# Performance work log

Measured on AMD Instinct MI355X. Metric: run time of the kernel, lower is better.

Reference implementation:

```python
import jax, jax.numpy as jnp
import numpy as np

# Dimensions (see shape_source)
B, D, Q, M = 2, 1024, 1024, 1024
K = Q + M                      # klen = mlen + qlen
N_HEAD, D_HEAD = 16, 64        # n_head * d_head == d_model
D_INNER = 4096
LOCAL_SIZE = 1000              # Attention: self.local_size or 1000
EPS = 1e-5                     # F.layer_norm default eps


def setup_inputs() -> dict:
    key = jax.random.key(0)
    ks = jax.random.split(key, 12)
    z = jax.random.normal(ks[0], (B, D, Q), jnp.float32)
    z_hist = jax.random.normal(ks[1], (B, D, M), jnp.float32)
    u = jax.random.normal(ks[2], (B, 3 * N_HEAD * D_HEAD, K), jnp.float32) * 0.1
    # sinusoidal relative position embedding (PositionalEmbedding), positions K-1..0
    inv_freq = 1.0 / (10000.0 ** (jnp.arange(0, D, 2, dtype=jnp.float32) / D))
    pos_seq = jnp.arange(K - 1, -1, -1, dtype=jnp.float32)
    sinusoid = inv_freq[:, None] * pos_seq[None, :]  # (D/2, K)
    pos_emb = jnp.concatenate([jnp.sin(sinusoid), jnp.cos(sinusoid)], axis=0)[None]  # (1, D, K)
    s = 0.02
    W_qkv = jax.random.normal(ks[3], (3 * N_HEAD * D_HEAD, D), jnp.float32) * s
    W_r = jax.random.normal(ks[4], (N_HEAD * D_HEAD, D), jnp.float32) * s
    r_w_bias = jax.random.uniform(ks[5], (N_HEAD, D_HEAD), jnp.float32, -0.05, 0.05)
    r_r_bias = jax.random.uniform(ks[6], (N_HEAD, D_HEAD), jnp.float32, -0.05, 0.05)
    W_o = jax.random.normal(ks[7], (D, N_HEAD * D_HEAD), jnp.float32) * s
    b_o = jnp.zeros((D,), jnp.float32)
    W_ff1 = jax.random.normal(ks[8], (D_INNER, D), jnp.float32) * s
    b_ff1 = jnp.zeros((D_INNER,), jnp.float32)
    W_ff2 = jax.random.normal(ks[9], (D, D_INNER), jnp.float32) * s
    b_ff2 = jnp.zeros((D,), jnp.float32)
    return dict(z=z, z_hist=z_hist, u=u, pos_emb=pos_emb, W_qkv=W_qkv, W_r=W_r,
                r_w_bias=r_w_bias, r_r_bias=r_r_bias, W_o=W_o, b_o=b_o,
                W_ff1=W_ff1, b_ff1=b_ff1, W_ff2=W_ff2, b_ff2=b_ff2)


def _ln(x, axis):
    # F.layer_norm without affine params
    mu = jnp.mean(x, axis=axis, keepdims=True)
    var = jnp.var(x, axis=axis, keepdims=True)
    return (x - mu) / jnp.sqrt(var + EPS)


def _rel_shift(x):
    # Transformer-XL relative shift: pad left on key dim, reinterpret, drop row.
    b, n, q, k = x.shape
    x = jnp.pad(x, ((0, 0), (0, 0), (0, 0), (1, 0)))
    x = x.reshape(b, n, k + 1, q)
    return x[:, :, 1:, :].reshape(b, n, q, k)


def reference(z, z_hist, u, pos_emb, W_qkv, W_r, r_w_bias, r_r_bias, W_o, b_o,
              W_ff1, b_ff1, W_ff2, b_ff2):
    scale = 1.0 / (D_HEAD ** 0.5)
    # ---- Attention (post-LN, Conv1d kernel=1 == pointwise matmul) ----
    cat = jnp.concatenate([z_hist, z], axis=2)                 # (B, D, K)
    w_heads = jnp.einsum('od,bdk->bok', W_qkv, cat) + u        # (B, 3*n*dh, K)
    q_h, k_h, v_h = jnp.split(w_heads, 3, axis=1)
    q_h = q_h[:, :, -Q:].reshape(B, N_HEAD, D_HEAD, Q)
    k_h = k_h.reshape(B, N_HEAD, D_HEAD, K)
    v_h = v_h.reshape(B, N_HEAD, D_HEAD, K)
    r_k = jnp.einsum('od,dk->ok', W_r, pos_emb[0]).reshape(N_HEAD, D_HEAD, K)
    AC = jnp.einsum('bndi,bndj->bnij', q_h + r_w_bias[:, :, None], k_h)
    BD = _rel_shift(jnp.einsum('bndi,ndj->bnij', q_h + r_r_bias[:, :, None], r_k))
    score = (AC + BD) * scale                                  # (B, n, Q, K)
    causal = jnp.triu(jnp.ones((Q, K), bool), k=1 + M)         # future tokens
    local = jnp.tril(jnp.ones((Q, K), bool), k=M - LOCAL_SIZE)  # beyond local window
    mask = causal | local
    score = jnp.where(mask[None, None], -jnp.inf, score)
    prob = jax.nn.softmax(score, axis=-1)
    attn_vec = jnp.einsum('bnij,bndj->bndi', prob, v_h).reshape(B, N_HEAD * D_HEAD, Q)
    attn_out = jnp.einsum('od,bdq->boq', W_o, attn_vec) + b_o[None, :, None]
    out = _ln(attn_out + z, axis=1)                            # LN over d_model (dim=1)
    # ---- FFN (operates token-major) ----
    h = out.transpose(0, 2, 1)                                 # (B, Q, D)
    ff = jnp.maximum(h @ W_ff1.T + b_ff1, 0.0) @ W_ff2.T + b_ff2
    y = _ln(ff + h, axis=-1)
    return y.transpose(0, 2, 1)                                # (B, D, Q)
```

## Files before the change

### kernel.cpp

```cpp
#include <hip/hip_runtime.h>

#define D_MODEL 1024
#define QLEN 1024

typedef __bf16 bf16x8 __attribute__((ext_vector_type(8)));
typedef __bf16 bf16x4 __attribute__((ext_vector_type(4)));
typedef float f32x4 __attribute__((ext_vector_type(4)));

__device__ __forceinline__ void gload16(const void* g, void* l) {
    __builtin_amdgcn_global_load_lds(
        (const __attribute__((address_space(1))) void*)g,
        (__attribute__((address_space(3))) void*)l, 16, 0, 0);
}

__device__ __forceinline__ void gemm_core8(
    __bf16* __restrict__ smA, __bf16* __restrict__ smB,
    const __bf16* __restrict__ A, const __bf16* __restrict__ Bt,
    float* __restrict__ C, __bf16* __restrict__ Cb,
    const float* __restrict__ U, const __bf16* __restrict__ Ub,
    const float* __restrict__ bias,
    int K, int lda, int ldb, int ldC, int ldU, int relu, int m0, int n0)
{
    const int t = threadIdx.x;
    const int lane = t & 63, w = t >> 6;
    const int l15 = lane & 15, lg = lane >> 4;
    const int wm = w >> 2, wn = w & 3;
    const int srow = lane >> 3, cpr = lane & 7;
    const int NK = K >> 6;
    const int SZ = 128 * 64;

    #define STAGE(buf, kt)                                                                   \
    {                                                                                        \
        int k0s = (kt) * 64;                                                                 \
        _Pragma("unroll")                                                                    \
        for (int i = 0; i < 2; ++i) {                                                        \
            int r = w * 16 + i * 8 + srow;                                                   \
            int c = cpr ^ (r & 7);                                                           \
            gload16(&A[(long long)(m0 + r) * lda + k0s + c * 8],                             \
                    &smA[(buf) * SZ + (w * 16 + i * 8) * 64]);                               \
            gload16(&Bt[(long long)(n0 + r) * ldb + k0s + c * 8],                            \
                    &smB[(buf) * SZ + (w * 16 + i * 8) * 64]);                               \
        }                                                                                    \
    }

    f32x4 acc[4][2] = {};
    STAGE(0, 0);

    for (int kt = 0; kt < NK; ++kt) {
        const int cb = kt & 1;
        if (kt + 1 < NK) {
            STAGE(cb ^ 1, kt + 1);
            asm volatile("s_waitcnt vmcnt(4)" ::: "memory");
        } else {
            asm volatile("s_waitcnt vmcnt(0)" ::: "memory");
        }
        __builtin_amdgcn_sched_barrier(0);
        __builtin_amdgcn_s_barrier();

        #pragma unroll
        for (int kk = 0; kk < 2; ++kk) {
            bf16x8 bfr[2];
            #pragma unroll
            for (int nt = 0; nt < 2; ++nt) {
                int nr = wn * 32 + nt * 16 + l15;
                bfr[nt] = *(const bf16x8*)&smB[cb * SZ + nr * 64 + (((kk * 4 + lg) ^ (nr & 7)) * 8)];
            }
            #pragma unroll
            for (int mt = 0; mt < 4; ++mt) {
                int mr = wm * 64 + mt * 16 + l15;
                bf16x8 afr = *(const bf16x8*)&smA[cb * SZ + mr * 64 + (((kk * 4 + lg) ^ (mr & 7)) * 8)];
                #pragma unroll
                for (int nt = 0; nt < 2; ++nt)
                    acc[mt][nt] = __builtin_amdgcn_mfma_f32_16x16x32_bf16(afr, bfr[nt], acc[mt][nt], 0, 0, 0);
            }
        }
        asm volatile("s_waitcnt lgkmcnt(0)" ::: "memory");
        __builtin_amdgcn_sched_barrier(0);
        __builtin_amdgcn_s_barrier();
    }
    #undef STAGE

    #pragma unroll
    for (int mt = 0; mt < 4; ++mt) {
        #pragma unroll
        for (int nt = 0; nt < 2; ++nt) {
            #pragma unroll
            for (int rg = 0; rg < 4; ++rg) {
                int m = m0 + wm * 64 + mt * 16 + lg * 4 + rg;
                int n = n0 + wn * 32 + nt * 16 + l15;
                float v = acc[mt][nt][rg];
                if (U)    v += U[(long long)m * ldU + n];
                if (Ub)   v += (float)Ub[(long long)m * ldU + n];
                if (bias) v += bias[n];
                if (relu) v = fmaxf(v, 0.0f);
                if (Cb) Cb[(long long)m * ldC + n] = (__bf16)v;
                else    C [(long long)m * ldC + n] = v;
            }
        }
    }
}

template<int KSPLIT>
__global__ __launch_bounds__(512) void gemm_bf16_k(
    const __bf16* __restrict__ A, const __bf16* __restrict__ Bt,
    float* __restrict__ C0, float* __restrict__ C1,
    float* __restrict__ C2, float* __restrict__ C3,
    __bf16* __restrict__ Cb,
    const float* __restrict__ U, const __bf16* __restrict__ Ub,
    const float* __restrict__ bias,
    int K, int lda, int ldb, int ldC, int ldU, int relu)
{
    __shared__ __bf16 SM[32768];
    int yb = blockIdx.y;
    int half = 0;
    if (KSPLIT > 1) { half = yb & (KSPLIT - 1); yb /= KSPLIT; }
    const int Keff = K / KSPLIT;
    A  += (long long)half * Keff;
    Bt += (long long)half * Keff;
    float* C = (half == 0) ? C0 : (half == 1) ? C1 : (half == 2) ? C2 : C3;
    if (half) { bias = nullptr; U = nullptr; Ub = nullptr; }
    gemm_core8(SM, SM + 16384, A, Bt, C, Cb, U, Ub, bias,
               Keff, lda, ldb, ldC, ldU, relu, yb * 128, blockIdx.x * 128);
}

__global__ __launch_bounds__(512) void gemm_fused3(
    const __bf16* __restrict__ cat_t, const __bf16* __restrict__ Wqkvb,
    __bf16* __restrict__ qkT, const __bf16* __restrict__ uqkT,
    __bf16* __restrict__ wh_v, const float* __restrict__ uv,
    const __bf16* __restrict__ pos_t, const __bf16* __restrict__ Wrb,
    __bf16* __restrict__ rkT)
{
    __shared__ __bf16 SM[32768];
    int bid = blockIdx.x;
    if (bid < 512) {
        int zz = bid >> 8, rem = bid & 255, y = rem >> 4, x = rem & 15;
        gemm_core8(SM, SM + 16384,
                   cat_t + (long long)zz * 2097152, Wqkvb,
                   nullptr, qkT + (long long)zz * 4194304,
                   nullptr, uqkT + (long long)zz * 4194304, nullptr,
                   1024, 1024, 1024, 2048, 2048, 0, y * 128, x * 128);
    } else if (bid < 768) {
        int l = bid - 512, zz = l >> 7, rem = l & 127, y = rem >> 4, x = rem & 15;
        gemm_core8(SM, SM + 16384,
                   Wqkvb + 2048 * 1024, cat_t + (long long)zz * 2097152,
                   nullptr, wh_v + (long long)zz * 2097152,
                   uv + (long long)zz * 6291456, nullptr, nullptr,
                   1024, 1024, 1024, 2048, 2048, 0, y * 128, x * 128);
    } else {
        int l = bid - 768, y = l >> 3, x = l & 7;
        gemm_core8(SM, SM + 16384,
                   pos_t + 960 * 1024, Wrb,
                   nullptr, rkT, nullptr, nullptr, nullptr,
                   1024, 1024, 1024, 1024, 0, 0, y * 128, x * 128);
    }
}

__global__ __launch_bounds__(256) void prep_all(
    const float* __restrict__ Wqkv, __bf16* __restrict__ Wqkvb,
    const float* __restrict__ Wr,   __bf16* __restrict__ Wrb,
    const float* __restrict__ Wo,   __bf16* __restrict__ Wob,
    const float* __restrict__ Wff1, __bf16* __restrict__ Wff1b,
    const float* __restrict__ Wff2, __bf16* __restrict__ Wff2b,
    const float* __restrict__ zh, const float* __restrict__ z, __bf16* __restrict__ cat_t,
    const float* __restrict__ pos, __bf16* __restrict__ pos_t,
    const float* __restrict__ u, __bf16* __restrict__ uqkT)
{
    __shared__ float ts[32][33];
    int bid = blockIdx.x;
    const int t = threadIdx.x;
    if (bid < 13312) {
        long long i = ((long long)bid * 256 + t) * 4;
        const float* s; __bf16* dd;
        if (i < 3145728)                    { s = Wqkv + i; dd = Wqkvb + i; }
        else if ((i -= 3145728) < 1048576)  { s = Wr + i;   dd = Wrb + i; }
        else if ((i -= 1048576) < 1048576)  { s = Wo + i;   dd = Wob + i; }
        else if ((i -= 1048576) < 4194304)  { s = Wff1 + i; dd = Wff1b + i; }
        else { i -= 4194304;                  s = Wff2 + i; dd = Wff2b + i; }
        float4 v = *(const float4*)s;
        bf16x4 o = { (__bf16)v.x, (__bf16)v.y, (__bf16)v.z, (__bf16)v.w };
        *(bf16x4*)dd = o;
        return;
    }
    bid -= 13312;
    const float* S; __bf16* D; int R, Cc, bx, by;
    if (bid < 2048) {
        int zz = bid >> 10, r2 = bid & 1023;
        S = zh + (long long)zz * 1048576; D = cat_t + (long long)zz * 2097152;
        R = 1024; Cc = 1024; bx = r2 & 31; by = r2 >> 5;
    } else if (bid < 4096) {
        int l = bid - 2048; int zz = l >> 10, r2 = l & 1023;
        S = z + (long long)zz * 1048576; D = cat_t + 1048576 + (long long)zz * 2097152;
        R = 1024; Cc = 1024; bx = r2 & 31; by = r2 >> 5;
    } else if (bid < 6144) {
        int l = bid - 4096;
        S = pos; D = pos_t; R = 1024; Cc = 2048; bx = l & 63; by = l >> 6;
    } else if (bid < 14336) {
        int l = bid - 6144; int zz = l >> 12, r2 = l & 4095;
        S = u + (long long)zz * 6291456; D = uqkT + (long long)zz * 4194304;
        R = 2048; Cc = 2048; bx = r2 & 63; by = r2 >> 6;
    } else {
        int l = bid - 14336;
        int i = (l * 256 + t) * 4;
        bf16x4 zv = { (__bf16)0.f, (__bf16)0.f, (__bf16)0.f, (__bf16)0.f };
        *(bf16x4*)&pos_t[2048 * 1024 + i] = zv;
        return;
    }
    int r0 = by * 32, c0 = bx * 32;
    int tr = t >> 5, tc = t & 31;
    #pragma unroll
    for (int p = 0; p < 4; ++p)
        ts[tr + p * 8][tc] = S[(long long)(r0 + tr + p * 8) * Cc + c0 + tc];
    __syncthreads();
    #pragma unroll
    for (int p = 0; p < 4; ++p)
        D[(long long)(c0 + tr + p * 8) * R + r0 + tc] = (__bf16)ts[tc][tr + p * 8];
}

__global__ __launch_bounds__(256) void attn_mfma(
    const __bf16* __restrict__ QKT, const __bf16* __restrict__ WHV,
    const __bf16* __restrict__ RKT,
    const float* __restrict__ rwb, const float* __restrict__ rrb,
    __bf16* __restrict__ AVt)
{
    __shared__ __bf16 SM[38144];
    __bf16* KT0 = SM;
    __bf16* KT1 = SM + 4096;
    __bf16* VS0 = SM + 8192;
    __bf16* VS1 = SM + 12288;
    __bf16* RT  = SM + 16384;
    __bf16* PS  = SM + 28672;
    __bf16* BT  = SM + 32768;

    const int d = blockIdx.x;
    const int xcd = d & 7, idx = d >> 3;
    const int qt = idx & 15;
    const int gq = xcd + 8 * (idx >> 4);
    const int b = gq >> 4, n = gq & 15;
    const int i0 = qt * 64;

    const int t = threadIdx.x;
    const int lane = t & 63, w = t >> 6;
    const int l15 = lane & 15, lg = lane >> 4;
    const int fco = n * 64;

    const __bf16* qkb = QKT + (long long)b * (2048 * 2048);
    const __bf16* vb  = WHV + (long long)b * (1024 * 2048) + (long long)fco * 2048;
    __bf16* BTw = BT + w * 1344;

    #pragma unroll
    for (int pp = 0; pp < 2; ++pp) {
        int cid = pp * 256 + t;
        int q = cid >> 3, s = cid & 7, c = s ^ (q & 7);
        bf16x8 qv = *(const bf16x8*)&qkb[(long long)(1024 + i0 + q) * 2048 + fco + c * 8];
        bf16x8 ow, orr;
        #pragma unroll
        for (int e = 0; e < 8; ++e) {
            float qf = (float)qv[e];
            ow[e]  = (__bf16)(qf + rwb[fco + c * 8 + e]);
            orr[e] = (__bf16)(qf + rrb[fco + c * 8 + e]);
        }
        *(bf16x8*)&PS[q * 64 + s * 8] = ow;
        *(bf16x8*)&VS0[q * 64 + s * 8] = orr;
    }
    __syncthreads();

    #define LDF(buf, row, ch) (*(const bf16x8*)&(buf)[(row) * 64 + ((((ch) ^ ((row) & 7))) * 8)])

    const int mrow = w * 16 + l15;
    bf16x8 qw0 = LDF(PS, mrow, lg), qw1 = LDF(PS, mrow, lg + 4);
    bf16x8 qr0 = LDF(VS0, mrow, lg), qr1 = LDF(VS0, mrow, lg + 4);
    asm volatile("s_waitcnt lgkmcnt(0)" ::: "memory");
    __builtin_amdgcn_sched_barrier(0);
    __builtin_amdgcn_s_barrier();

    #pragma unroll
    for (int pp = 0; pp < 2; ++pp) {
        int cid = pp * 256 + t;
        int r = cid >> 3, s = cid & 7, c = s ^ (r & 7);
        gload16(&qkb[(long long)(i0 + r) * 2048 + 1024 + fco + c * 8], &KT0[(pp * 32 + w * 8) * 64]);
        gload16(&vb[(long long)r * 2048 + i0 + c * 8], &VS0[(pp * 32 + w * 8) * 64]);
    }
    #pragma unroll
    for (int pp = 0; pp < 6; ++pp) {
        int cid = pp * 256 + t;
        int r = cid >> 3, s = cid & 7, c = s ^ (r & 7);
        gload16(&RKT[(long long)r * 1024 + fco + c * 8], &RT[(pp * 32 + w * 8) * 64]);
    }
    asm volatile("s_waitcnt vmcnt(0)" ::: "memory");
    __builtin_amdgcn_sched_barrier(0);
    __builtin_amdgcn_s_barrier();

    const bf16x8 ones = { (__bf16)1.f, (__bf16)1.f, (__bf16)1.f, (__bf16)1.f,
                          (__bf16)1.f, (__bf16)1.f, (__bf16)1.f, (__bf16)1.f };

    f32x4 O0 = {}, O1 = {}, O2 = {}, O3 = {};
    float rm[4] = {-1e30f, -1e30f, -1e30f, -1e30f};
    float rl[4] = {0.f, 0.f, 0.f, 0.f};
    int cur = 0;

    for (int kt = 0; kt <= 16; ++kt) {
        __bf16* KTc = cur ? KT1 : KT0;
        __bf16* VSc = cur ? VS1 : VS0;
        __bf16* KTn = cur ? KT0 : KT1;
        __bf16* VSn = cur ? VS0 : VS1;
        const int rbase = (kt % 3) * 64;

        if (kt < 16) {
            int j0n = i0 + (kt + 1) * 64;
            #pragma unroll
            for (int pp = 0; pp < 2; ++pp) {
                int cid = pp * 256 + t;
                int r = cid >> 3, s = cid & 7, c = s ^ (r & 7);
                gload16(&qkb[(long long)(j0n + r) * 2048 + 1024 + fco + c * 8], &KTn[(pp * 32 + w * 8) * 64]);
                gload16(&vb[(long long)r * 2048 + j0n + c * 8], &VSn[(pp * 32 + w * 8) * 64]);
            }
            int rb = kt * 64 + 128;
            int lb = ((kt + 2) % 3) * 64;
            #pragma unroll
            for (int pp = 0; pp < 2; ++pp) {
                int cid = pp * 256 + t;
                int r = cid >> 3, s = cid & 7, c = s ^ (r & 7);
                gload16(&RKT[(long long)(rb + r) * 1024 + fco + c * 8], &RT[(lb + pp * 32 + w * 8) * 64]);
            }
        }
        __builtin_amdgcn_sched_barrier(0);

        __builtin_amdgcn_s_setprio(1);
        #pragma unroll
        for (int k5 = 0; k5 < 5; ++k5) {
            int pr = (3 - w + k5) * 16 + l15;
            int lr = rbase + pr; if (lr >= 192) lr -= 192;
            const __bf16* rrow = &RT[lr * 64];
            f32x4 cc = {};
            cc = __builtin_amdgcn_mfma_f32_16x16x32_bf16(qr0, *(const bf16x8*)&rrow[((lg ^ (pr & 7)) * 8)], cc, 0, 0, 0);
            cc = __builtin_amdgcn_mfma_f32_16x16x32_bf16(qr1, *(const bf16x8*)&rrow[(((lg + 4) ^ (pr & 7)) * 8)], cc, 0, 0, 0);
            #pragma unroll
            for (int rg = 0; rg < 4; ++rg)
                BTw[(lg * 4 + rg) * 84 + k5 * 16 + l15] = (__bf16)cc[rg];
        }
        __builtin_amdgcn_s_setprio(0);

        f32x4 cc4[4];
        __builtin_amdgcn_s_setprio(1);
        #pragma unroll
        for (int nt = 0; nt < 4; ++nt) {
            int jr = nt * 16 + l15;
            f32x4 cc = {};
            cc = __builtin_amdgcn_mfma_f32_16x16x32_bf16(qw0, LDF(KTc, jr, lg), cc, 0, 0, 0);
            cc = __builtin_amdgcn_mfma_f32_16x16x32_bf16(qw1, LDF(KTc, jr, lg + 4), cc, 0, 0, 0);
            cc4[nt] = cc;
        }
        __builtin_amdgcn_s_setprio(0);

        const bool bnd = (kt < 2) | (kt == 16);
        float sv[4][4];
        if (!bnd) {
            #pragma unroll
            for (int nt = 0; nt < 4; ++nt) {
                int jr = nt * 16 + l15;
                #pragma unroll
                for (int rg = 0; rg < 4; ++rg) {
                    int r4 = lg * 4 + rg;
                    sv[nt][rg] = (cc4[nt][rg] + (float)BTw[r4 * 84 + jr - r4 + 15]) * 0.125f;
                }
            }
        } else {
            #pragma unroll
            for (int nt = 0; nt < 4; ++nt) {
                int jr = nt * 16 + l15;
                #pragma unroll
                for (int rg = 0; rg < 4; ++rg) {
                    int r4 = lg * 4 + rg;
                    int dji = jr - (w * 16 + r4);
                    float s = (cc4[nt][rg] + (float)BTw[r4 * 84 + jr - r4 + 15]) * 0.125f;
                    bool valid = (kt == 0) ? (dji >= 25)
                               : (kt == 1) ? (dji >= -39)
                               : (dji <= 0);
                    sv[nt][rg] = valid ? s : -1e30f;
                }
            }
        }

        float lmax[4];
        bool need = false;
        #pragma unroll
        for (int rg = 0; rg < 4; ++rg) {
            lmax[rg] = fmaxf(fmaxf(sv[0][rg], sv[1][rg]), fmaxf(sv[2][rg], sv[3][rg]));
            need = need || (lmax[rg] > rm[rg] + 8.0f);
        }
        if (__any(need)) {
            #pragma unroll
            for (int rg = 0; rg < 4; ++rg) {
                float m = lmax[rg];
                m = fmaxf(m, __shfl_xor(m, 1, 16));
                m = fmaxf(m, __shfl_xor(m, 2, 16));
                m = fmaxf(m, __shfl_xor(m, 4, 16));
                m = fmaxf(m, __shfl_xor(m, 8, 16));
                float nm = fmaxf(rm[rg], m);
                float fac = __expf(rm[rg] - nm);
                rm[rg] = nm;
                rl[rg] *= fac;
                O0[rg] *= fac; O1[rg] *= fac; O2[rg] *= fac; O3[rg] *= fac;
            }
        }

        if (!bnd) {
            #pragma unroll
            for (int nt = 0; nt < 4; ++nt) {
                int jc = nt * 16 + l15;
                #pragma unroll
                for (int rg = 0; rg < 4; ++rg) {
                    float p = __expf(sv[nt][rg] - rm[rg]);
                    int row = w * 16 + lg * 4 + rg;
                    PS[row * 64 + (((jc >> 3) ^ (row & 7)) * 8) + (jc & 7)] = (__bf16)p;
                }
            }
        } else {
            #pragma unroll
            for (int nt = 0; nt < 4; ++nt) {
                int jc = nt * 16 + l15;
                #pragma unroll
                for (int rg = 0; rg < 4; ++rg) {
                    float p = (sv[nt][rg] > -1e29f) ? __expf(sv[nt][rg] - rm[rg]) : 0.0f;
                    int row = w * 16 + lg * 4 + rg;
                    PS[row * 64 + (((jc >> 3) ^ (row & 7)) * 8) + (jc & 7)] = (__bf16)p;
                }
            }
        }

        bf16x8 pa0 = LDF(PS, mrow, lg), pa1 = LDF(PS, mrow, lg + 4);
        f32x4 Os = {};
        __builtin_amdgcn_s_setprio(1);
        Os = __builtin_amdgcn_mfma_f32_16x16x32_bf16(pa0, ones, Os, 0, 0, 0);
        Os = __builtin_amdgcn_mfma_f32_16x16x32_bf16(pa1, ones, Os, 0, 0, 0);
        O0 = __builtin_amdgcn_mfma_f32_16x16x32_bf16(pa0, LDF(VSc,  0 + l15, lg),     O0, 0, 0, 0);
        O0 = __builtin_amdgcn_mfma_f32_16x16x32_bf16(pa1, LDF(VSc,  0 + l15, lg + 4), O0, 0, 0, 0);
        O1 = __builtin_amdgcn_mfma_f32_16x16x32_bf16(pa0, LDF(VSc, 16 + l15, lg),     O1, 0, 0, 0);
        O1 = __builtin_amdgcn_mfma_f32_16x16x32_bf16(pa1, LDF(VSc, 16 + l15, lg + 4), O1, 0, 0, 0);
        O2 = __builtin_amdgcn_mfma_f32_16x16x32_bf16(pa0, LDF(VSc, 32 + l15, lg),     O2, 0, 0, 0);
        O2 = __builtin_amdgcn_mfma_f32_16x16x32_bf16(pa1, LDF(VSc, 32 + l15, lg + 4), O2, 0, 0, 0);
        O3 = __builtin_amdgcn_mfma_f32_16x16x32_bf16(pa0, LDF(VSc, 48 + l15, lg),     O3, 0, 0, 0);
        O3 = __builtin_amdgcn_mfma_f32_16x16x32_bf16(pa1, LDF(VSc, 48 + l15, lg + 4), O3, 0, 0, 0);
        __builtin_amdgcn_s_setprio(0);
        #pragma unroll
        for (int rg = 0; rg < 4; ++rg) rl[rg] += Os[rg];

        asm volatile("s_waitcnt vmcnt(0)" ::: "memory");
        __builtin_amdgcn_sched_barrier(0);
        __builtin_amdgcn_s_barrier();
        cur ^= 1;
    }

    #pragma unroll
    for (int rg = 0; rg < 4; ++rg) {
        float inv = 1.0f / rl[rg];
        int q = i0 + w * 16 + lg * 4 + rg;
        long long base = ((long long)b * 1024 + q) * 1024 + fco;
        AVt[base +  0 + l15] = (__bf16)(O0[rg] * inv);
        AVt[base + 16 + l15] = (__bf16)(O1[rg] * inv);
        AVt[base + 32 + l15] = (__bf16)(O2[rg] * inv);
        AVt[base + 48 + l15] = (__bf16)(O3[rg] * inv);
    }
    #undef LDF
}

__global__ __launch_bounds__(256) void ln1_kernel(
    const float* __restrict__ A0, const float* __restrict__ A1,
    const float* __restrict__ A2, const float* __restrict__ A3,
    const float* __restrict__ bo, const __bf16* __restrict__ CatT,
    __bf16* __restrict__ Hb)
{
    int i = blockIdx.x, b = blockIdx.y, t = threadIdx.x;
    __shared__ float xs[D_MODEL];
    __shared__ float red[256];
    __shared__ float smu, srstd;
    long long tb = ((long long)b * 1024 + i) * 1024;
    long long zb = ((long long)b * 2048 + 1024 + i) * 1024;

    float lsum = 0.0f;
    for (int dd = t; dd < D_MODEL; dd += 256) {
        float v = A0[tb + dd] + A1[tb + dd] + A2[tb + dd] + A3[tb + dd]
                + bo[dd] + (float)CatT[zb + dd];
        xs[dd] = v;
        lsum += v;
    }
    red[t] = lsum; __syncthreads();
    for (int s2 = 128; s2 > 0; s2 >>= 1) { if (t < s2) red[t] += red[t + s2]; __syncthreads(); }
    if (t == 0) smu = red[0] * (1.0f / D_MODEL);
    __syncthreads();
    float mu = smu;

    float lq = 0.0f;
    for (int dd = t; dd < D_MODEL; dd += 256) { float c = xs[dd] - mu; lq += c * c; }
    red[t] = lq; __syncthreads();
    for (int s2 = 128; s2 > 0; s2 >>= 1) { if (t < s2) red[t] += red[t + s2]; __syncthreads(); }
    if (t == 0) srstd = rsqrtf(red[0] * (1.0f / D_MODEL) + 1e-5f);
    __syncthreads();
    float rstd = srstd;

    for (int dd = t; dd < D_MODEL; dd += 256)
        Hb[tb + dd] = (__bf16)((xs[dd] - mu) * rstd);
}

__global__ __launch_bounds__(256) void ln2_stats(
    const float* __restrict__ F0, const float* __restrict__ F1,
    const float* __restrict__ F2p, const float* __restrict__ F3,
    const __bf16* __restrict__ Hb, float2* __restrict__ st)
{
    int i = blockIdx.x, b = blockIdx.y, t = threadIdx.x;
    __shared__ float rs[256], rq[256];
    long long tb = ((long long)b * 1024 + i) * 1024;

    float s = 0.f, q = 0.f;
    for (int dd = t; dd < D_MODEL; dd += 256) {
        float v = F0[tb + dd] + F1[tb + dd] + F2p[tb + dd] + F3[tb + dd] + (float)Hb[tb + dd];
        s += v; q += v * v;
    }
    rs[t] = s; rq[t] = q; __syncthreads();
    for (int s2 = 128; s2 > 0; s2 >>= 1) {
        if (t < s2) { rs[t] += rs[t + s2]; rq[t] += rq[t + s2]; }
        __syncthreads();
    }
    if (t == 0) {
        float mu = rs[0] * (1.0f / D_MODEL);
        float var = rq[0] * (1.0f / D_MODEL) - mu * mu;
        st[(long long)b * 1024 + i] = make_float2(mu, rsqrtf(var + 1e-5f));
    }
}

__global__ __launch_bounds__(256) void ln2_write(
    const float* __restrict__ F0, const float* __restrict__ F1,
    const float* __restrict__ F2p, const float* __restrict__ F3,
    const __bf16* __restrict__ Hb, const float2* __restrict__ st,
    float* __restrict__ OUT)
{
    __shared__ float ts[32][33];
    int f0 = blockIdx.x * 32, i0 = blockIdx.y * 32, b = blockIdx.z;
    int tr = threadIdx.x >> 5, tc = threadIdx.x & 31;
    #pragma unroll
    for (int p = 0; p < 4; ++p) {
        int tok = i0 + tr + p * 8;
        long long tb = ((long long)b * 1024 + tok) * 1024;
        float2 s = st[(long long)b * 1024 + tok];
        float v = F0[tb + f0 + tc] + F1[tb + f0 + tc] + F2p[tb + f0 + tc] + F3[tb + f0 + tc]
                + (float)Hb[tb + f0 + tc];
        ts[tr + p * 8][tc] = (v - s.x) * s.y;
    }
    __syncthreads();
    #pragma unroll
    for (int p = 0; p < 4; ++p)
        OUT[((long long)b * 1024 + f0 + tr + p * 8) * 1024 + i0 + tc] = ts[tc][tr + p * 8];
}

extern "C" void kernel_launch(void* const* d_in, const int* in_sizes, int n_in,
                              void* d_out, int out_size, void* d_ws, size_t ws_size,
                              hipStream_t stream) {
    const float* z    = (const float*)d_in[0];
    const float* zh   = (const float*)d_in[1];
    const float* u    = (const float*)d_in[2];
    const float* pos  = (const float*)d_in[3];
    const float* Wqkv = (const float*)d_in[4];
    const float* Wr   = (const float*)d_in[5];
    const float* rwb  = (const float*)d_in[6];
    const float* rrb  = (const float*)d_in[7];
    const float* Wo   = (const float*)d_in[8];
    const float* bo   = (const float*)d_in[9];
    const float* Wff1 = (const float*)d_in[10];
    const float* bff1 = (const float*)d_in[11];
    const float* Wff2 = (const float*)d_in[12];
    const float* bff2 = (const float*)d_in[13];
    float* out = (float*)d_out;
    float* ws  = (float*)d_ws;

    __bf16* cat_t = (__bf16*)ws;
    __bf16* pos_t = (__bf16*)(ws + 2097152);
    __bf16* Wqkvb = (__bf16*)(ws + 3178496);
    __bf16* Wrb   = (__bf16*)(ws + 4751360);
    __bf16* Wob   = (__bf16*)(ws + 5275648);
    __bf16* Wff1b = (__bf16*)(ws + 5799936);
    __bf16* Wff2b = (__bf16*)(ws + 7897088);
    __bf16* uqkT  = (__bf16*)(ws + 9994240);
    __bf16* qkT   = (__bf16*)(ws + 14188544);
    __bf16* wh_v  = (__bf16*)(ws + 18382848);
    __bf16* rkT   = (__bf16*)(ws + 20480000);
    __bf16* av_t  = (__bf16*)(ws + 21069824);
    float*  ao0   = ws + 22118400;
    float*  ao1   = ws + 24215552;
    float*  ao2   = ws + 14188544;
    float*  ao3   = ws + 16285696;
    __bf16* h_bf  = (__bf16*)(ws + 26312704);
    float2* st2   = (float2*)(ws + 27361280);
    __bf16* f1b   = (__bf16*)(ws + 14188544);
    float*  f20   = ws + 9994240;
    float*  f21   = ws + 12091392;
    float*  f22   = ws + 18382848;
    float*  f23   = ws + 22118400;

    prep_all<<<27712, 256, 0, stream>>>(
        Wqkv, Wqkvb, Wr, Wrb, Wo, Wob, Wff1, Wff1b, Wff2, Wff2b,
        zh, z, cat_t, pos, pos_t, u, uqkT);

    gemm_fused3<<<840, 512, 0, stream>>>(
        cat_t, Wqkvb, qkT, uqkT, wh_v, u + 4194304, pos_t, Wrb, rkT);

    attn_mfma<<<512, 256, 0, stream>>>(qkT, wh_v, rkT, rwb, rrb, av_t);

    gemm_bf16_k<4><<<dim3(8, 64, 1), 512, 0, stream>>>(
        av_t, Wob, ao0, ao1, ao2, ao3, nullptr, nullptr, nullptr, nullptr,
        1024, 1024, 1024, 1024, 0, 0);
    ln1_kernel<<<dim3(1024, 2), 256, 0, stream>>>(ao0, ao1, ao2, ao3, bo, cat_t, h_bf);
    gemm_bf16_k<1><<<dim3(32, 16, 1), 512, 0, stream>>>(
        h_bf, Wff1b, nullptr, nullptr, nullptr, nullptr, f1b, nullptr, nullptr, bff1,
        1024, 1024, 1024, 4096, 0, 1);
    gemm_bf16_k<4><<<dim3(8, 64, 1), 512, 0, stream>>>(
        f1b, Wff2b, f20, f21, f22, f23, nullptr, nullptr, nullptr, bff2,
        4096, 4096, 4096, 1024, 0, 0);
    ln2_stats<<<dim3(1024, 2), 256, 0, stream>>>(f20, f21, f22, f23, h_bf, st2);
    ln2_write<<<dim3(32, 32, 2), 256, 0, stream>>>(f20, f21, f22, f23, h_bf, st2, out);
}
```

Measured before the change: 224.0 us.

## Read u transposed in GEMM epilogue and halve split-K partial buffers

Drops the prep pass that transposed u's q/k slice into a bf16 buffer. The fused QKV GEMM epilogue now reads u directly in fp32 with transposed indexing. Split-K for the output projection and FFN2 goes from 4 to 2, so the LN kernels read two partial buffers instead of four. This saves a large transpose pass and partial-sum traffic, but the epilogue reads u with a strided pattern and the split-K GEMMs launch half as many blocks.

```diff
diff --git a/kernel.cpp b/kernel.cpp
--- a/kernel.cpp
+++ b/kernel.cpp
@@ -17,7 +17,7 @@
     __bf16* __restrict__ smA, __bf16* __restrict__ smB,
     const __bf16* __restrict__ A, const __bf16* __restrict__ Bt,
     float* __restrict__ C, __bf16* __restrict__ Cb,
-    const float* __restrict__ U, const __bf16* __restrict__ Ub,
+    const float* __restrict__ U, const float* __restrict__ Ut,
     const float* __restrict__ bias,
     int K, int lda, int ldb, int ldC, int ldU, int relu, int m0, int n0)
 {
@@ -90,7 +90,7 @@
                 int n = n0 + wn * 32 + nt * 16 + l15;
                 float v = acc[mt][nt][rg];
                 if (U)    v += U[(long long)m * ldU + n];
-                if (Ub)   v += (float)Ub[(long long)m * ldU + n];
+                if (Ut)   v += Ut[(long long)n * ldU + m];
                 if (bias) v += bias[n];
                 if (relu) v = fmaxf(v, 0.0f);
                 if (Cb) Cb[(long long)m * ldC + n] = (__bf16)v;
@@ -104,10 +104,8 @@
 __global__ __launch_bounds__(512) void gemm_bf16_k(
     const __bf16* __restrict__ A, const __bf16* __restrict__ Bt,
     float* __restrict__ C0, float* __restrict__ C1,
-    float* __restrict__ C2, float* __restrict__ C3,
     __bf16* __restrict__ Cb,
-    const float* __restrict__ U, const __bf16* __restrict__ Ub,
-    const float* __restrict__ bias,
+    const float* __restrict__ U, const float* __restrict__ bias,
     int K, int lda, int ldb, int ldC, int ldU, int relu)
 {
     __shared__ __bf16 SM[32768];
@@ -117,16 +115,16 @@
     const int Keff = K / KSPLIT;
     A  += (long long)half * Keff;
     Bt += (long long)half * Keff;
-    float* C = (half == 0) ? C0 : (half == 1) ? C1 : (half == 2) ? C2 : C3;
-    if (half) { bias = nullptr; U = nullptr; Ub = nullptr; }
-    gemm_core8(SM, SM + 16384, A, Bt, C, Cb, U, Ub, bias,
+    float* C = half ? C1 : C0;
+    if (half) { bias = nullptr; U = nullptr; }
+    gemm_core8(SM, SM + 16384, A, Bt, C, Cb, U, nullptr, bias,
                Keff, lda, ldb, ldC, ldU, relu, yb * 128, blockIdx.x * 128);
 }
 
 __global__ __launch_bounds__(512) void gemm_fused3(
     const __bf16* __restrict__ cat_t, const __bf16* __restrict__ Wqkvb,
-    __bf16* __restrict__ qkT, const __bf16* __restrict__ uqkT,
-    __bf16* __restrict__ wh_v, const float* __restrict__ uv,
+    __bf16* __restrict__ qkT, const float* __restrict__ u,
+    __bf16* __restrict__ wh_v,
     const __bf16* __restrict__ pos_t, const __bf16* __restrict__ Wrb,
     __bf16* __restrict__ rkT)
 {
@@ -137,14 +135,14 @@
         gemm_core8(SM, SM + 16384,
                    cat_t + (long long)zz * 2097152, Wqkvb,
                    nullptr, qkT + (long long)zz * 4194304,
-                   nullptr, uqkT + (long long)zz * 4194304, nullptr,
+                   nullptr, u + (long long)zz * 6291456, nullptr,
                    1024, 1024, 1024, 2048, 2048, 0, y * 128, x * 128);
     } else if (bid < 768) {
         int l = bid - 512, zz = l >> 7, rem = l & 127, y = rem >> 4, x = rem & 15;
         gemm_core8(SM, SM + 16384,
                    Wqkvb + 2048 * 1024, cat_t + (long long)zz * 2097152,
                    nullptr, wh_v + (long long)zz * 2097152,
-                   uv + (long long)zz * 6291456, nullptr, nullptr,
+                   u + 4194304 + (long long)zz * 6291456, nullptr, nullptr,
                    1024, 1024, 1024, 2048, 2048, 0, y * 128, x * 128);
     } else {
         int l = bid - 768, y = l >> 3, x = l & 7;
@@ -162,8 +160,7 @@
     const float* __restrict__ Wff1, __bf16* __restrict__ Wff1b,
     const float* __restrict__ Wff2, __bf16* __restrict__ Wff2b,
     const float* __restrict__ zh, const float* __restrict__ z, __bf16* __restrict__ cat_t,
-    const float* __restrict__ pos, __bf16* __restrict__ pos_t,
-    const float* __restrict__ u, __bf16* __restrict__ uqkT)
+    const float* __restrict__ pos, __bf16* __restrict__ pos_t)
 {
     __shared__ float ts[32][33];
     int bid = blockIdx.x;
@@ -194,12 +191,8 @@
     } else if (bid < 6144) {
         int l = bid - 4096;
         S = pos; D = pos_t; R = 1024; Cc = 2048; bx = l & 63; by = l >> 6;
-    } else if (bid < 14336) {
-        int l = bid - 6144; int zz = l >> 12, r2 = l & 4095;
-        S = u + (long long)zz * 6291456; D = uqkT + (long long)zz * 4194304;
-        R = 2048; Cc = 2048; bx = r2 & 63; by = r2 >> 6;
     } else {
-        int l = bid - 14336;
+        int l = bid - 6144;
         int i = (l * 256 + t) * 4;
         bf16x4 zv = { (__bf16)0.f, (__bf16)0.f, (__bf16)0.f, (__bf16)0.f };
         *(bf16x4*)&pos_t[2048 * 1024 + i] = zv;
@@ -466,7 +459,6 @@
 
 __global__ __launch_bounds__(256) void ln1_kernel(
     const float* __restrict__ A0, const float* __restrict__ A1,
-    const float* __restrict__ A2, const float* __restrict__ A3,
     const float* __restrict__ bo, const __bf16* __restrict__ CatT,
     __bf16* __restrict__ Hb)
 {
@@ -479,8 +471,7 @@
 
     float lsum = 0.0f;
     for (int dd = t; dd < D_MODEL; dd += 256) {
-        float v = A0[tb + dd] + A1[tb + dd] + A2[tb + dd] + A3[tb + dd]
-                + bo[dd] + (float)CatT[zb + dd];
+        float v = A0[tb + dd] + A1[tb + dd] + bo[dd] + (float)CatT[zb + dd];
         xs[dd] = v;
         lsum += v;
     }
@@ -504,7 +495,6 @@
 
 __global__ __launch_bounds__(256) void ln2_stats(
     const float* __restrict__ F0, const float* __restrict__ F1,
-    const float* __restrict__ F2p, const float* __restrict__ F3,
     const __bf16* __restrict__ Hb, float2* __restrict__ st)
 {
     int i = blockIdx.x, b = blockIdx.y, t = threadIdx.x;
@@ -513,7 +503,7 @@
 
     float s = 0.f, q = 0.f;
     for (int dd = t; dd < D_MODEL; dd += 256) {
-        float v = F0[tb + dd] + F1[tb + dd] + F2p[tb + dd] + F3[tb + dd] + (float)Hb[tb + dd];
+        float v = F0[tb + dd] + F1[tb + dd] + (float)Hb[tb + dd];
         s += v; q += v * v;
     }
     rs[t] = s; rq[t] = q; __syncthreads();
@@ -530,7 +520,6 @@
 
 __global__ __launch_bounds__(256) void ln2_write(
     const float* __restrict__ F0, const float* __restrict__ F1,
-    const float* __restrict__ F2p, const float* __restrict__ F3,
     const __bf16* __restrict__ Hb, const float2* __restrict__ st,
     float* __restrict__ OUT)
 {
@@ -542,8 +531,7 @@
         int tok = i0 + tr + p * 8;
         long long tb = ((long long)b * 1024 + tok) * 1024;
         float2 s = st[(long long)b * 1024 + tok];
-        float v = F0[tb + f0 + tc] + F1[tb + f0 + tc] + F2p[tb + f0 + tc] + F3[tb + f0 + tc]
-                + (float)Hb[tb + f0 + tc];
+        float v = F0[tb + f0 + tc] + F1[tb + f0 + tc] + (float)Hb[tb + f0 + tc];
         ts[tr + p * 8][tc] = (v - s.x) * s.y;
     }
     __syncthreads();
@@ -579,42 +567,37 @@
     __bf16* Wob   = (__bf16*)(ws + 5275648);
     __bf16* Wff1b = (__bf16*)(ws + 5799936);
     __bf16* Wff2b = (__bf16*)(ws + 7897088);
-    __bf16* uqkT  = (__bf16*)(ws + 9994240);
     __bf16* qkT   = (__bf16*)(ws + 14188544);
     __bf16* wh_v  = (__bf16*)(ws + 18382848);
     __bf16* rkT   = (__bf16*)(ws + 20480000);
     __bf16* av_t  = (__bf16*)(ws + 21069824);
     float*  ao0   = ws + 22118400;
     float*  ao1   = ws + 24215552;
-    float*  ao2   = ws + 14188544;
-    float*  ao3   = ws + 16285696;
     __bf16* h_bf  = (__bf16*)(ws + 26312704);
     float2* st2   = (float2*)(ws + 27361280);
     __bf16* f1b   = (__bf16*)(ws + 14188544);
     float*  f20   = ws + 9994240;
     float*  f21   = ws + 12091392;
-    float*  f22   = ws + 18382848;
-    float*  f23   = ws + 22118400;
-
-    prep_all<<<27712, 256, 0, stream>>>(
+
+    prep_all<<<19520, 256, 0, stream>>>(
         Wqkv, Wqkvb, Wr, Wrb, Wo, Wob, Wff1, Wff1b, Wff2, Wff2b,
-        zh, z, cat_t, pos, pos_t, u, uqkT);
+        zh, z, cat_t, pos, pos_t);
 
     gemm_fused3<<<840, 512, 0, stream>>>(
-        cat_t, Wqkvb, qkT, uqkT, wh_v, u + 4194304, pos_t, Wrb, rkT);
+        cat_t, Wqkvb, qkT, u, wh_v, pos_t, Wrb, rkT);
 
     attn_mfma<<<512, 256, 0, stream>>>(qkT, wh_v, rkT, rwb, rrb, av_t);
 
-    gemm_bf16_k<4><<<dim3(8, 64, 1), 512, 0, stream>>>(
-        av_t, Wob, ao0, ao1, ao2, ao3, nullptr, nullptr, nullptr, nullptr,
+    gemm_bf16_k<2><<<dim3(8, 32, 1), 512, 0, stream>>>(
+        av_t, Wob, ao0, ao1, nullptr, nullptr, nullptr,
         1024, 1024, 1024, 1024, 0, 0);
-    ln1_kernel<<<dim3(1024, 2), 256, 0, stream>>>(ao0, ao1, ao2, ao3, bo, cat_t, h_bf);
+    ln1_kernel<<<dim3(1024, 2), 256, 0, stream>>>(ao0, ao1, bo, cat_t, h_bf);
     gemm_bf16_k<1><<<dim3(32, 16, 1), 512, 0, stream>>>(
-        h_bf, Wff1b, nullptr, nullptr, nullptr, nullptr, f1b, nullptr, nullptr, bff1,
+        h_bf, Wff1b, nullptr, nullptr, f1b, nullptr, bff1,
         1024, 1024, 1024, 4096, 0, 1);
-    gemm_bf16_k<4><<<dim3(8, 64, 1), 512, 0, stream>>>(
-        f1b, Wff2b, f20, f21, f22, f23, nullptr, nullptr, nullptr, bff2,
+    gemm_bf16_k<2><<<dim3(8, 32, 1), 512, 0, stream>>>(
+        f1b, Wff2b, f20, f21, nullptr, nullptr, bff2,
         4096, 4096, 4096, 1024, 0, 0);
-    ln2_stats<<<dim3(1024, 2), 256, 0, stream>>>(f20, f21, f22, f23, h_bf, st2);
-    ln2_write<<<dim3(32, 32, 2), 256, 0, stream>>>(f20, f21, f22, f23, h_bf, st2, out);
-}
+    ln2_stats<<<dim3(1024, 2), 256, 0, stream>>>(f20, f21, h_bf, st2);
+    ln2_write<<<dim3(32, 32, 2), 256, 0, stream>>>(f20, f21, h_bf, st2, out);
+}
```

Result: faster. 214.1 us (-4.4%).
